# Performance work log

Hardware: AMD Instinct MI355X
Metric: run time of the kernel (lower is better)

## Reference

```python
import jax, jax.numpy as jnp
import numpy as np

N_NODES = 50000


def gcn_conv(x, edge_index, W, b):
    """GCNConv with added self-loops and symmetric D^-1/2 (A+I) D^-1/2 normalization."""
    n = x.shape[0]
    h = x @ W  # [N, out]
    loop = jnp.arange(n, dtype=edge_index.dtype)
    src = jnp.concatenate([edge_index[0], loop])
    dst = jnp.concatenate([edge_index[1], loop])
    ones = jnp.ones(src.shape[0], dtype=x.dtype)
    deg = jax.ops.segment_sum(ones, dst, num_segments=n)  # in-degree incl. self-loop
    dis = jnp.where(deg > 0, jax.lax.rsqrt(deg), 0.0).astype(x.dtype)
    norm = dis[src] * dis[dst]  # [E+N]
    msg = h[src] * norm[:, None]  # gather + scale
    out = jax.ops.segment_sum(msg, dst, num_segments=n)  # scatter-add
    return out + b


def setup_inputs() -> dict:
    key = jax.random.key(0)
    ks = jax.random.split(key, 6)
    d_in, d_h, d_out = 256, 256, 128
    x = jax.random.normal(ks[0], (N_NODES, d_in), dtype=jnp.float32)
    edge_index = jax.random.randint(ks[1], (2, 1600000), 0, N_NODES, dtype=jnp.int64)
    edge_label_index = jax.random.randint(ks[2], (2, 100000), 0, N_NODES, dtype=jnp.int64)
    W1 = jax.random.normal(ks[3], (d_in, d_h), dtype=jnp.float32) * (1.0 / np.sqrt(d_in))
    b1 = jnp.zeros((d_h,), dtype=jnp.float32)
    W2 = jax.random.normal(ks[4], (d_h, d_out), dtype=jnp.float32) * (1.0 / np.sqrt(d_h))
    b2 = jnp.zeros((d_out,), dtype=jnp.float32)
    return {"x": x, "edge_index": edge_index, "edge_label_index": edge_label_index,
            "W1": W1, "b1": b1, "W2": W2, "b2": b2}


def reference(x, edge_index, edge_label_index, W1, b1, W2, b2):
    # encode (eval mode: dropout is identity)
    z = jax.nn.relu(gcn_conv(x, edge_index, W1, b1))
    z = gcn_conv(z, edge_index, W2, b2)  # [N, 128]
    # decode: gather endpoint embeddings and reduce (edge dot-product scores)
    y = jnp.sum(z[edge_label_index[0]] * z[edge_label_index[1]], axis=-1)  # [E_label]
    return y
```

## Files before the change

### kernel.cpp

```cpp
#include <hip/hip_runtime.h>
#include <hip/hip_bf16.h>


#define CH 4096

typedef __attribute__((ext_vector_type(8))) short short8;
typedef __attribute__((ext_vector_type(4))) float f32x4;
typedef __attribute__((ext_vector_type(4))) unsigned int u32x4;

__device__ __forceinline__ unsigned short f2bf_rne(float f) {
  unsigned int b = __float_as_uint(f);
  b += 0x7FFFu + ((b >> 16) & 1u);
  return (unsigned short)(b >> 16);
}
__device__ __forceinline__ float u8f_0(unsigned int r) { return (float)(r & 255u); }
__device__ __forceinline__ float u8f_1(unsigned int r) { return (float)((r >> 8) & 255u); }
__device__ __forceinline__ float u8f_2(unsigned int r) { return (float)((r >> 16) & 255u); }
__device__ __forceinline__ float u8f_3(unsigned int r) { return (float)(r >> 24); }

__device__ __forceinline__ int dim1_of(int p) {
  return ((p >> 7) << 7) + (((p >> 6) & 1) << 6) + ((p >> 2) & 15) + ((p & 3) << 4);
}

__launch_bounds__(256) __global__
void prep_k(const float* __restrict__ W1, unsigned short* __restrict__ W1t,
            const float* __restrict__ W2, unsigned short* __restrict__ W2t,
            int* __restrict__ gcnt) {
  int t = threadIdx.x, b = blockIdx.x;
  if (b == 0) gcnt[t] = 0;
  int j = b * 256 + t;
  const int m1 = 256 * 256;
  if (j < m1) {
    int k = j >> 8, c = j & 255;
    W1t[(size_t)c * 256 + k] = f2bf_rne(W1[j]);
  } else if (j < m1 + 128 * 256) {
    int j2 = j - m1;
    int c = j2 >> 8, p = j2 & 255;
    W2t[(size_t)c * 256 + p] = f2bf_rne(W2[(size_t)dim1_of(p) * 128 + c]);
  }
}

#define LDST 40
template <bool AF32, int QROWW, bool DISFOLD>
__device__ __forceinline__
void gemm_body(const void* __restrict__ Av, const unsigned short* __restrict__ Bt,
               unsigned int* __restrict__ Q, float* __restrict__ wsout,
               const float* __restrict__ dis, int M, int N, int K, int bx, int by,
               short* As, short* Bs, float (*rm)[2]) {
  int t = threadIdx.x;
  int lane = t & 63, wave = t >> 6;
  int quad = lane >> 4, l16 = lane & 15;
  int wm = (wave & 1) * 64, wn = (wave >> 1) * 64;
  int wn6 = wn >> 6;
  int m0 = by * 128, n0 = bx * 128;

  int row0 = t >> 2, c80 = (t & 3) * 8;
  int row1 = row0 + 64, c81 = c80;
  int gr0 = m0 + row0, gr1 = m0 + row1;

  f32x4 acc[4][4];
#pragma unroll
  for (int i = 0; i < 4; i++)
#pragma unroll
    for (int j = 0; j < 4; j++) acc[i][j] = (f32x4)0.f;

  float4 fa00, fa01, fa10, fa11;
  uint4 ua0, ua1;
  uint4 ub0, ub1;

  auto load_tile = [&](int k0) {
    if (AF32) {
      const float* A = (const float*)Av;
      fa00 = make_float4(0.f, 0.f, 0.f, 0.f); fa01 = fa00; fa10 = fa00; fa11 = fa00;
      if (gr0 < M) {
        fa00 = *reinterpret_cast<const float4*>(A + (size_t)gr0 * K + k0 + c80);
        fa01 = *reinterpret_cast<const float4*>(A + (size_t)gr0 * K + k0 + c80 + 4);
      }
      if (gr1 < M) {
        fa10 = *reinterpret_cast<const float4*>(A + (size_t)gr1 * K + k0 + c81);
        fa11 = *reinterpret_cast<const float4*>(A + (size_t)gr1 * K + k0 + c81 + 4);
      }
    } else {
      const unsigned short* A = (const unsigned short*)Av;
      ua0 = make_uint4(0u, 0u, 0u, 0u); ua1 = ua0;
      if (gr0 < M) ua0 = *reinterpret_cast<const uint4*>(A + (size_t)gr0 * K + k0 + c80);
      if (gr1 < M) ua1 = *reinterpret_cast<const uint4*>(A + (size_t)gr1 * K + k0 + c81);
    }
    ub0 = *reinterpret_cast<const uint4*>(Bt + (size_t)(n0 + row0) * K + k0 + c80);
    ub1 = *reinterpret_cast<const uint4*>(Bt + (size_t)(n0 + row1) * K + k0 + c81);
  };

  load_tile(0);
  for (int k0 = 0; k0 < K; k0 += 32) {
    __syncthreads();
    uint4 av0, av1;
    if (AF32) {
      av0.x = (unsigned)f2bf_rne(fa00.x) | ((unsigned)f2bf_rne(fa00.y) << 16);
      av0.y = (unsigned)f2bf_rne(fa00.z) | ((unsigned)f2bf_rne(fa00.w) << 16);
      av0.z = (unsigned)f2bf_rne(fa01.x) | ((unsigned)f2bf_rne(fa01.y) << 16);
      av0.w = (unsigned)f2bf_rne(fa01.z) | ((unsigned)f2bf_rne(fa01.w) << 16);
      av1.x = (unsigned)f2bf_rne(fa10.x) | ((unsigned)f2bf_rne(fa10.y) << 16);
      av1.y = (unsigned)f2bf_rne(fa10.z) | ((unsigned)f2bf_rne(fa10.w) << 16);
      av1.z = (unsigned)f2bf_rne(fa11.x) | ((unsigned)f2bf_rne(fa11.y) << 16);
      av1.w = (unsigned)f2bf_rne(fa11.z) | ((unsigned)f2bf_rne(fa11.w) << 16);
    } else {
      av0 = ua0; av1 = ua1;
    }
    *reinterpret_cast<uint4*>(&As[row0 * LDST + c80]) = av0;
    *reinterpret_cast<uint4*>(&Bs[row0 * LDST + c80]) = ub0;
    *reinterpret_cast<uint4*>(&As[row1 * LDST + c81]) = av1;
    *reinterpret_cast<uint4*>(&Bs[row1 * LDST + c81]) = ub1;
    __syncthreads();
    if (k0 + 32 < K) load_tile(k0 + 32);
    short8 af[4], bfr[4];
#pragma unroll
    for (int mt = 0; mt < 4; mt++)
      af[mt] = *reinterpret_cast<const short8*>(&As[(wm + mt * 16 + l16) * LDST + quad * 8]);
#pragma unroll
    for (int nt = 0; nt < 4; nt++)
      bfr[nt] = *reinterpret_cast<const short8*>(&Bs[(wn + nt * 16 + l16) * LDST + quad * 8]);
#pragma unroll
    for (int mt = 0; mt < 4; mt++)
#pragma unroll
      for (int nt = 0; nt < 4; nt++)
        acc[mt][nt] = __builtin_amdgcn_mfma_f32_16x16x32_bf16(af[mt], bfr[nt], acc[mt][nt], 0, 0, 0);
  }

#pragma unroll
  for (int mt = 0; mt < 4; mt++) {
#pragma unroll
    for (int r = 0; r < 4; r++) {
      float m = fmaxf(fmaxf(fabsf(acc[mt][0][r]), fabsf(acc[mt][1][r])),
                      fmaxf(fabsf(acc[mt][2][r]), fabsf(acc[mt][3][r])));
#pragma unroll
      for (int off = 1; off < 16; off <<= 1) m = fmaxf(m, __shfl_xor(m, off));
      if (l16 == 0) rm[wm + mt * 16 + quad * 4 + r][wn6] = m;
    }
  }
  __syncthreads();
#pragma unroll
  for (int mt = 0; mt < 4; mt++) {
#pragma unroll
    for (int r = 0; r < 4; r++) {
      int rl = wm + mt * 16 + quad * 4 + r;
      int grow = m0 + rl;
      if (grow >= M) continue;
      float mx = fmaxf(rm[rl][0], rm[rl][1]);
      float inv = mx > 0.f ? 127.f / mx : 0.f;
      unsigned int uq[4];
#pragma unroll
      for (int nt = 0; nt < 4; nt++) {
        int tq = (int)rintf(acc[mt][nt][r] * inv);
        tq = tq > 127 ? 127 : (tq < -127 ? -127 : tq);
        uq[nt] = (unsigned int)(tq + 128);
      }
      unsigned int pk = uq[0] | (uq[1] << 8) | (uq[2] << 16) | (uq[3] << 24);
      int qcol = (QROWW == 64 ? (n0 >> 7) * 32 : 0) + wn6 * 16 + l16;
      Q[(size_t)grow * QROWW + qcol] = pk;
      if (wn6 == 0 && l16 == 0) {
        float sc = mx * (1.f / 127.f);
        if (DISFOLD) sc *= dis[grow];
        if (QROWW == 64) wsout[grow * 2 + (n0 >> 7)] = sc;
        else wsout[grow] = sc;
      }
    }
  }
}

__launch_bounds__(256) __global__
void fat1_k(const float* __restrict__ x, const unsigned short* __restrict__ W1t,
            unsigned int* __restrict__ Q, float* __restrict__ rawsc,
            int M, int N, int K, int NG,
            const int* __restrict__ src, const int* __restrict__ dst,
            int* __restrict__ gcnt, unsigned int* __restrict__ rec,
            int E, int BCAP) {
  __shared__ short As[128 * LDST];
  __shared__ short Bs[128 * LDST];
  __shared__ float rm[128][2];
  int bid = blockIdx.x;
  int t = threadIdx.x;
  if (bid < NG) {
    gemm_body<true, 64, false>(x, W1t, Q, rawsc, nullptr, M, N, K,
                               bid & 1, bid >> 1, As, Bs, rm);
    return;
  }
  int* h = (int*)As;
  int* ofs = h + 256;
  int* c2 = ofs + 256;
  int b = bid - NG;
  h[t] = 0;
  c2[t] = 0;
  __syncthreads();
  int i0 = b * CH, i1 = i0 + CH;
  if (i1 > E) i1 = E;
  for (int i = i0 + t; i < i1; i += 256) {
    int d = __builtin_nontemporal_load(&dst[i]);
    atomicAdd(&h[d >> 8], 1);
  }
  __syncthreads();
  {
    int cb = h[t];
    int base = atomicAdd(&gcnt[t], cb);
    ofs[t] = t * BCAP + base;
  }
  __syncthreads();
  int lim_base = 0;
  (void)lim_base;
  for (int i = i0 + t; i < i1; i += 256) {
    int d = __builtin_nontemporal_load(&dst[i]);
    int s = __builtin_nontemporal_load(&src[i]);
    int bk = d >> 8;
    int r = atomicAdd(&c2[bk], 1);
    int pos = ofs[bk] + r;
    if (pos < (bk + 1) * BCAP)
      rec[(size_t)pos] = ((unsigned int)(d & 255) << 16) | (unsigned int)s;
  }
}

__launch_bounds__(256) __global__
void sort2_dis_k(const unsigned int* __restrict__ rec, const int* __restrict__ gcnt,
                 unsigned short* __restrict__ edges, int* __restrict__ rowst,
                 int* __restrict__ fill, float* __restrict__ dis,
                 float* __restrict__ ws1, int n, int BCAP) {
  __shared__ int hist[256], scanv[256], c2[256];
  int t = threadIdx.x, b = blockIdx.x;
  int nrec = gcnt[b];
  if (nrec > BCAP) nrec = BCAP;
  size_t bs = (size_t)b * BCAP;
  hist[t] = 0;
  __syncthreads();
  const unsigned int* rp = rec + bs;
  for (int i = t; i < nrec; i += 256) atomicAdd(&hist[rp[i] >> 16], 1);
  __syncthreads();
  if (t == 0) {
    int s = 0;
    for (int k = 0; k < 256; k++) { scanv[k] = s; s += hist[k]; }
  }
  __syncthreads();
  int d = b * 256 + t;
  if (d < n) {
    fill[d] = hist[t];
    rowst[d] = (int)bs + scanv[t];
    float dv = rsqrtf((float)(hist[t] + 1));
    dis[d] = dv;
    ws1[2 * d] *= dv;
    ws1[2 * d + 1] *= dv;
  }
  c2[t] = 0;
  __syncthreads();
  for (int i = t; i < nrec; i += 256) {
    unsigned int r = rp[i];
    int dl = (int)(r >> 16);
    int pos = scanv[dl] + atomicAdd(&c2[dl], 1);
    edges[bs + pos] = (unsigned short)r;
  }
}

__launch_bounds__(256) __global__
void gemmq2_k(const unsigned short* __restrict__ A, const unsigned short* __restrict__ Bt,
              unsigned int* __restrict__ Q, float* __restrict__ wsout,
              const float* __restrict__ dis, int M, int N, int K) {
  __shared__ short As[128 * LDST];
  __shared__ short Bs[128 * LDST];
  __shared__ float rm[128][2];
  gemm_body<false, 32, true>(A, Bt, Q, wsout, dis, M, N, K, 0, blockIdx.x, As, Bs, rm);
}

template <int VEC, bool RELU, bool OBF, bool WS2>
__launch_bounds__(256) __global__
void aggregate_k(const void* __restrict__ qv, const int* __restrict__ fill,
                 const int* __restrict__ rowst, const unsigned short* __restrict__ edges,
                 const float* __restrict__ ws, const float* __restrict__ dis,
                 const float* __restrict__ bias, void* __restrict__ outv, int n) {
  const int DIM = VEC * 64;
  int wave = threadIdx.x >> 6, lane = threadIdx.x & 63;
  int node = blockIdx.x * (blockDim.x >> 6) + wave;
  if (node >= n) return;
  int start = rowst[node], end = start + fill[node];
  float di = dis[node];
  int hsel = lane >> 5;
  float bv[VEC];
  if (VEC == 4) {
    int base = (hsel << 7) + (((lane >> 4) & 1) << 6) + (lane & 15);
#pragma unroll
    for (int v = 0; v < 4; v++) bv[v] = bias[base + (v << 4)];
  } else {
    int c0 = (hsel << 6) + ((lane >> 1) & 15) + ((lane & 1) << 5);
    bv[0] = bias[c0];
    bv[1] = bias[c0 + 16];
  }
  const unsigned int* q4 = (const unsigned int*)qv;
  const unsigned short* q2 = (const unsigned short*)qv;
  float acc[VEC];
  float sw;
  {
    float w = WS2 ? ws[2 * node + hsel] : ws[node];
    sw = w;
    if (VEC == 4) {
      unsigned int r = q4[(size_t)node * 64 + lane];
      acc[0] = u8f_0(r) * w; acc[1] = u8f_1(r) * w;
      acc[2] = u8f_2(r) * w; acc[3] = u8f_3(r) * w;
    } else {
      unsigned int r = q2[(size_t)node * 64 + lane];
      acc[0] = u8f_0(r) * w; acc[1] = u8f_1(r) * w;
    }
  }
  int e = start;
  for (; e < end && (e & 7); e++) {
    unsigned int s = edges[e];
    float w = WS2 ? ws[2 * s + hsel] : ws[s];
    sw += w;
    if (VEC == 4) {
      unsigned int r = q4[(size_t)s * 64 + lane];
      acc[0] = fmaf(u8f_0(r), w, acc[0]);
      acc[1] = fmaf(u8f_1(r), w, acc[1]);
      acc[2] = fmaf(u8f_2(r), w, acc[2]);
      acc[3] = fmaf(u8f_3(r), w, acc[3]);
    } else {
      unsigned int r = q2[(size_t)s * 64 + lane];
      acc[0] = fmaf(u8f_0(r), w, acc[0]);
      acc[1] = fmaf(u8f_1(r), w, acc[1]);
    }
  }
  for (; e + 8 <= end; e += 8) {
    u32x4 ev = __builtin_nontemporal_load(reinterpret_cast<const u32x4*>(&edges[e]));
    unsigned int s[8];
    s[0] = ev.x & 0xFFFFu; s[1] = ev.x >> 16;
    s[2] = ev.y & 0xFFFFu; s[3] = ev.y >> 16;
    s[4] = ev.z & 0xFFFFu; s[5] = ev.z >> 16;
    s[6] = ev.w & 0xFFFFu; s[7] = ev.w >> 16;
    float w[8];
#pragma unroll
    for (int j = 0; j < 8; j++) w[j] = WS2 ? ws[2 * s[j] + hsel] : ws[s[j]];
#pragma unroll
    for (int j = 0; j < 8; j++) sw += w[j];
    if (VEC == 4) {
      unsigned int r[8];
#pragma unroll
      for (int j = 0; j < 8; j++) r[j] = q4[(size_t)s[j] * 64 + lane];
#pragma unroll
      for (int j = 0; j < 8; j++) {
        acc[0] = fmaf(u8f_0(r[j]), w[j], acc[0]);
        acc[1] = fmaf(u8f_1(r[j]), w[j], acc[1]);
        acc[2] = fmaf(u8f_2(r[j]), w[j], acc[2]);
        acc[3] = fmaf(u8f_3(r[j]), w[j], acc[3]);
      }
    } else {
      unsigned int r[8];
#pragma unroll
      for (int j = 0; j < 8; j++) r[j] = q2[(size_t)s[j] * 64 + lane];
#pragma unroll
      for (int j = 0; j < 8; j++) {
        acc[0] = fmaf(u8f_0(r[j]), w[j], acc[0]);
        acc[1] = fmaf(u8f_1(r[j]), w[j], acc[1]);
      }
    }
  }
  for (; e < end; e++) {
    unsigned int s = edges[e];
    float w = WS2 ? ws[2 * s + hsel] : ws[s];
    sw += w;
    if (VEC == 4) {
      unsigned int r = q4[(size_t)s * 64 + lane];
      acc[0] = fmaf(u8f_0(r), w, acc[0]);
      acc[1] = fmaf(u8f_1(r), w, acc[1]);
      acc[2] = fmaf(u8f_2(r), w, acc[2]);
      acc[3] = fmaf(u8f_3(r), w, acc[3]);
    } else {
      unsigned int r = q2[(size_t)s * 64 + lane];
      acc[0] = fmaf(u8f_0(r), w, acc[0]);
      acc[1] = fmaf(u8f_1(r), w, acc[1]);
    }
  }
  float corr = 128.f * sw;
#pragma unroll
  for (int v = 0; v < VEC; v++) {
    float r = fmaf(di, acc[v] - corr, bv[v]);
    if (RELU) r = fmaxf(r, 0.f);
    acc[v] = r;
  }
  if (OBF) {
    unsigned short* op = (unsigned short*)outv + (size_t)node * DIM + lane * VEC;
    if (VEC == 4) {
      unsigned int p0 = (unsigned int)f2bf_rne(acc[0]) | ((unsigned int)f2bf_rne(acc[1]) << 16);
      unsigned int p1 = (unsigned int)f2bf_rne(acc[2]) | ((unsigned int)f2bf_rne(acc[3]) << 16);
      *reinterpret_cast<uint2*>(op) = make_uint2(p0, p1);
    } else {
      unsigned int p0 = (unsigned int)f2bf_rne(acc[0]) | ((unsigned int)f2bf_rne(acc[1]) << 16);
      *reinterpret_cast<unsigned int*>(op) = p0;
    }
  } else {
    float* op = (float*)outv + (size_t)node * DIM + lane * VEC;
#pragma unroll
    for (int v = 0; v < VEC; v++) op[v] = acc[v];
  }
}

__launch_bounds__(256) __global__
void decode_k(const float* __restrict__ z, const int* __restrict__ ea,
              const int* __restrict__ eb, float* __restrict__ y, int E) {
  int wave = threadIdx.x >> 6, lane = threadIdx.x & 63;
  int e = blockIdx.x * (blockDim.x >> 6) + wave;
  if (e >= E) return;
  int a = ea[e], b = eb[e];
  const float2* za = reinterpret_cast<const float2*>(z + (size_t)a * 128);
  const float2* zb = reinterpret_cast<const float2*>(z + (size_t)b * 128);
  float2 pa = za[lane], pb = zb[lane];
  float s = pa.x * pb.x + pa.y * pb.y;
#pragma unroll
  for (int off = 32; off; off >>= 1) s += __shfl_down(s, off);
  if (lane == 0) y[e] = s;
}

extern "C" void kernel_launch(void* const* d_in, const int* in_sizes, int n_in,
                              void* d_out, int out_size, void* d_ws, size_t ws_size,
                              hipStream_t stream) {
  const float* x = (const float*)d_in[0];
  const int* ei = (const int*)d_in[1];
  const int* eli = (const int*)d_in[2];
  const float* W1 = (const float*)d_in[3];
  const float* b1 = (const float*)d_in[4];
  const float* W2 = (const float*)d_in[5];
  const float* b2 = (const float*)d_in[6];
  float* y = (float*)d_out;

  const int DIN = 256, DH = 256, DOUT = 128;
  const int n = in_sizes[0] / DIN;
  const int E = in_sizes[1] / 2;
  const int EL = in_sizes[2] / 2;
  const int* src = ei;
  const int* dst = ei + E;
  const int* ea = eli;
  const int* eb = eli + EL;

  const int NB = (E + CH - 1) / CH;
  const int NBUCK = (n + 255) / 256;
  const int PB = (DIN * DH + DH * DOUT + 255) / 256;
  const int MB = (n + 127) / 128;
  const int NG = 2 * MB;
  const int BCAP = 10240;

  size_t off = 0;
  auto alloc = [&](size_t bytes) {
    void* p = (char*)d_ws + off;
    off += (bytes + 255) & ~(size_t)255;
    return p;
  };
  int* fill = (int*)alloc((size_t)n * 4);
  int* rowst = (int*)alloc((size_t)n * 4);
  int* gcnt = (int*)alloc((size_t)256 * 4);
  unsigned int* rec = (unsigned int*)alloc((size_t)256 * BCAP * 4);
  float* dis = (float*)alloc((size_t)n * 4);
  float* ws2 = (float*)alloc((size_t)n * 2 * 4);
  float* wsB = (float*)alloc((size_t)n * 4);
  unsigned short* edges = (unsigned short*)alloc((size_t)256 * BCAP * 2);
  unsigned short* W1t = (unsigned short*)alloc((size_t)DIN * DH * 2);
  unsigned short* W2t = (unsigned short*)alloc((size_t)DH * DOUT * 2);
  unsigned int* qbuf = (unsigned int*)alloc((size_t)n * 64 * 4);
  unsigned short* z1b = (unsigned short*)alloc((size_t)n * DH * 2);
  float* z2 = (float*)alloc((size_t)n * DOUT * 4);
  (void)ws_size;

  prep_k<<<PB, 256, 0, stream>>>(W1, W1t, W2, W2t, gcnt);
  fat1_k<<<NG + NB, 256, 0, stream>>>(x, W1t, qbuf, ws2, n, DH, DIN, NG,
                                      src, dst, gcnt, rec, E, BCAP);
  sort2_dis_k<<<NBUCK, 256, 0, stream>>>(rec, gcnt, edges, rowst, fill, dis, ws2, n, BCAP);
  aggregate_k<4, true, true, true><<<(n + 3) / 4, 256, 0, stream>>>(
      qbuf, fill, rowst, edges, ws2, dis, b1, z1b, n);
  gemmq2_k<<<MB, 256, 0, stream>>>(z1b, W2t, qbuf, wsB, dis, n, DOUT, DH);
  aggregate_k<2, false, false, false><<<(n + 3) / 4, 256, 0, stream>>>(
      qbuf, fill, rowst, edges, wsB, dis, b2, z2, n);
  decode_k<<<(EL + 3) / 4, 256, 0, stream>>>(z2, ea, eb, y, EL);
}
```

Measured before the change: 341.7 us.

## Fuse all GCN stages into one persistent cooperative kernel with grid syncs

Replaces the seven separate kernel launches with a single cooperative persistent kernel that loops over each stage's work items and separates the stages with grid-wide barriers. The aim is to remove the per-launch overhead and the idle gaps between dependent kernels. The cost is fewer resident blocks, since occupancy is capped by the GEMM's shared-memory and register needs in every phase. Grid barriers also serialise the stages, and the old multi-kernel path is kept as a fallback if the cooperative launch fails.

```diff
diff --git a/kernel.cpp b/kernel.cpp
--- a/kernel.cpp
+++ b/kernel.cpp
@@ -1,5 +1,6 @@
 #include <hip/hip_runtime.h>
 #include <hip/hip_bf16.h>
+#include <hip/hip_cooperative_groups.h>
 
 
 #define CH 4096
@@ -20,6 +21,423 @@
 
 __device__ __forceinline__ int dim1_of(int p) {
   return ((p >> 7) << 7) + (((p >> 6) & 1) << 6) + ((p >> 2) & 15) + ((p & 3) << 4);
+}
+
+#define LDST 40
+template <bool AF32, int QROWW, bool DISFOLD>
+__device__ __forceinline__
+void gemm_body(const void* __restrict__ Av, const unsigned short* __restrict__ Bt,
+               unsigned int* __restrict__ Q, float* __restrict__ wsout,
+               const float* __restrict__ dis, int M, int N, int K, int bx, int by,
+               short* As, short* Bs, float (*rm)[2]) {
+  int t = threadIdx.x;
+  int lane = t & 63, wave = t >> 6;
+  int quad = lane >> 4, l16 = lane & 15;
+  int wm = (wave & 1) * 64, wn = (wave >> 1) * 64;
+  int wn6 = wn >> 6;
+  int m0 = by * 128, n0 = bx * 128;
+
+  int row0 = t >> 2, c80 = (t & 3) * 8;
+  int row1 = row0 + 64, c81 = c80;
+  int gr0 = m0 + row0, gr1 = m0 + row1;
+
+  f32x4 acc[4][4];
+#pragma unroll
+  for (int i = 0; i < 4; i++)
+#pragma unroll
+    for (int j = 0; j < 4; j++) acc[i][j] = (f32x4)0.f;
+
+  float4 fa00, fa01, fa10, fa11;
+  uint4 ua0, ua1;
+  uint4 ub0, ub1;
+
+  auto load_tile = [&](int k0) {
+    if (AF32) {
+      const float* A = (const float*)Av;
+      fa00 = make_float4(0.f, 0.f, 0.f, 0.f); fa01 = fa00; fa10 = fa00; fa11 = fa00;
+      if (gr0 < M) {
+        fa00 = *reinterpret_cast<const float4*>(A + (size_t)gr0 * K + k0 + c80);
+        fa01 = *reinterpret_cast<const float4*>(A + (size_t)gr0 * K + k0 + c80 + 4);
+      }
+      if (gr1 < M) {
+        fa10 = *reinterpret_cast<const float4*>(A + (size_t)gr1 * K + k0 + c81);
+        fa11 = *reinterpret_cast<const float4*>(A + (size_t)gr1 * K + k0 + c81 + 4);
+      }
+    } else {
+      const unsigned short* A = (const unsigned short*)Av;
+      ua0 = make_uint4(0u, 0u, 0u, 0u); ua1 = ua0;
+      if (gr0 < M) ua0 = *reinterpret_cast<const uint4*>(A + (size_t)gr0 * K + k0 + c80);
+      if (gr1 < M) ua1 = *reinterpret_cast<const uint4*>(A + (size_t)gr1 * K + k0 + c81);
+    }
+    ub0 = *reinterpret_cast<const uint4*>(Bt + (size_t)(n0 + row0) * K + k0 + c80);
+    ub1 = *reinterpret_cast<const uint4*>(Bt + (size_t)(n0 + row1) * K + k0 + c81);
+  };
+
+  load_tile(0);
+  for (int k0 = 0; k0 < K; k0 += 32) {
+    __syncthreads();
+    uint4 av0, av1;
+    if (AF32) {
+      av0.x = (unsigned)f2bf_rne(fa00.x) | ((unsigned)f2bf_rne(fa00.y) << 16);
+      av0.y = (unsigned)f2bf_rne(fa00.z) | ((unsigned)f2bf_rne(fa00.w) << 16);
+      av0.z = (unsigned)f2bf_rne(fa01.x) | ((unsigned)f2bf_rne(fa01.y) << 16);
+      av0.w = (unsigned)f2bf_rne(fa01.z) | ((unsigned)f2bf_rne(fa01.w) << 16);
+      av1.x = (unsigned)f2bf_rne(fa10.x) | ((unsigned)f2bf_rne(fa10.y) << 16);
+      av1.y = (unsigned)f2bf_rne(fa10.z) | ((unsigned)f2bf_rne(fa10.w) << 16);
+      av1.z = (unsigned)f2bf_rne(fa11.x) | ((unsigned)f2bf_rne(fa11.y) << 16);
+      av1.w = (unsigned)f2bf_rne(fa11.z) | ((unsigned)f2bf_rne(fa11.w) << 16);
+    } else {
+      av0 = ua0; av1 = ua1;
+    }
+    *reinterpret_cast<uint4*>(&As[row0 * LDST + c80]) = av0;
+    *reinterpret_cast<uint4*>(&Bs[row0 * LDST + c80]) = ub0;
+    *reinterpret_cast<uint4*>(&As[row1 * LDST + c81]) = av1;
+    *reinterpret_cast<uint4*>(&Bs[row1 * LDST + c81]) = ub1;
+    __syncthreads();
+    if (k0 + 32 < K) load_tile(k0 + 32);
+    short8 af[4], bfr[4];
+#pragma unroll
+    for (int mt = 0; mt < 4; mt++)
+      af[mt] = *reinterpret_cast<const short8*>(&As[(wm + mt * 16 + l16) * LDST + quad * 8]);
+#pragma unroll
+    for (int nt = 0; nt < 4; nt++)
+      bfr[nt] = *reinterpret_cast<const short8*>(&Bs[(wn + nt * 16 + l16) * LDST + quad * 8]);
+#pragma unroll
+    for (int mt = 0; mt < 4; mt++)
+#pragma unroll
+      for (int nt = 0; nt < 4; nt++)
+        acc[mt][nt] = __builtin_amdgcn_mfma_f32_16x16x32_bf16(af[mt], bfr[nt], acc[mt][nt], 0, 0, 0);
+  }
+
+#pragma unroll
+  for (int mt = 0; mt < 4; mt++) {
+#pragma unroll
+    for (int r = 0; r < 4; r++) {
+      float m = fmaxf(fmaxf(fabsf(acc[mt][0][r]), fabsf(acc[mt][1][r])),
+                      fmaxf(fabsf(acc[mt][2][r]), fabsf(acc[mt][3][r])));
+#pragma unroll
+      for (int off = 1; off < 16; off <<= 1) m = fmaxf(m, __shfl_xor(m, off));
+      if (l16 == 0) rm[wm + mt * 16 + quad * 4 + r][wn6] = m;
+    }
+  }
+  __syncthreads();
+#pragma unroll
+  for (int mt = 0; mt < 4; mt++) {
+#pragma unroll
+    for (int r = 0; r < 4; r++) {
+      int rl = wm + mt * 16 + quad * 4 + r;
+      int grow = m0 + rl;
+      if (grow >= M) continue;
+      float mx = fmaxf(rm[rl][0], rm[rl][1]);
+      float inv = mx > 0.f ? 127.f / mx : 0.f;
+      unsigned int uq[4];
+#pragma unroll
+      for (int nt = 0; nt < 4; nt++) {
+        int tq = (int)rintf(acc[mt][nt][r] * inv);
+        tq = tq > 127 ? 127 : (tq < -127 ? -127 : tq);
+        uq[nt] = (unsigned int)(tq + 128);
+      }
+      unsigned int pk = uq[0] | (uq[1] << 8) | (uq[2] << 16) | (uq[3] << 24);
+      int qcol = (QROWW == 64 ? (n0 >> 7) * 32 : 0) + wn6 * 16 + l16;
+      Q[(size_t)grow * QROWW + qcol] = pk;
+      if (wn6 == 0 && l16 == 0) {
+        float sc = mx * (1.f / 127.f);
+        if (DISFOLD) sc *= dis[grow];
+        if (QROWW == 64) wsout[grow * 2 + (n0 >> 7)] = sc;
+        else wsout[grow] = sc;
+      }
+    }
+  }
+}
+
+__device__ __forceinline__
+void scat_body(int b, const int* __restrict__ src, const int* __restrict__ dst,
+               int* __restrict__ gcnt, unsigned int* __restrict__ rec,
+               int E, int BCAP, int* lds) {
+  int t = threadIdx.x;
+  int* h = lds;
+  int* ofs = lds + 256;
+  int* c2 = lds + 512;
+  __syncthreads();
+  h[t] = 0;
+  c2[t] = 0;
+  __syncthreads();
+  int i0 = b * CH, i1 = i0 + CH;
+  if (i1 > E) i1 = E;
+  for (int i = i0 + t; i < i1; i += 256) {
+    int d = __builtin_nontemporal_load(&dst[i]);
+    atomicAdd(&h[d >> 8], 1);
+  }
+  __syncthreads();
+  {
+    int cb = h[t];
+    int base = atomicAdd(&gcnt[t], cb);
+    ofs[t] = t * BCAP + base;
+  }
+  __syncthreads();
+  for (int i = i0 + t; i < i1; i += 256) {
+    int d = __builtin_nontemporal_load(&dst[i]);
+    int s = __builtin_nontemporal_load(&src[i]);
+    int bk = d >> 8;
+    int r = atomicAdd(&c2[bk], 1);
+    int pos = ofs[bk] + r;
+    if (pos < (bk + 1) * BCAP)
+      rec[(size_t)pos] = ((unsigned int)(d & 255) << 16) | (unsigned int)s;
+  }
+}
+
+__device__ __forceinline__
+void sort2_body(int b, const unsigned int* __restrict__ rec, const int* __restrict__ gcnt,
+                unsigned short* __restrict__ edges, int* __restrict__ rowst,
+                int* __restrict__ fill, float* __restrict__ dis,
+                float* __restrict__ ws1, int n, int BCAP, int* lds) {
+  int t = threadIdx.x;
+  int* hist = lds;
+  int* scanv = lds + 256;
+  int* c2 = lds + 512;
+  int nrec = gcnt[b];
+  if (nrec > BCAP) nrec = BCAP;
+  size_t bs = (size_t)b * BCAP;
+  __syncthreads();
+  hist[t] = 0;
+  __syncthreads();
+  const unsigned int* rp = rec + bs;
+  for (int i = t; i < nrec; i += 256) atomicAdd(&hist[rp[i] >> 16], 1);
+  __syncthreads();
+  if (t == 0) {
+    int s = 0;
+    for (int k = 0; k < 256; k++) { scanv[k] = s; s += hist[k]; }
+  }
+  __syncthreads();
+  int d = b * 256 + t;
+  if (d < n) {
+    fill[d] = hist[t];
+    rowst[d] = (int)bs + scanv[t];
+    float dv = rsqrtf((float)(hist[t] + 1));
+    dis[d] = dv;
+    ws1[2 * d] *= dv;
+    ws1[2 * d + 1] *= dv;
+  }
+  c2[t] = 0;
+  __syncthreads();
+  for (int i = t; i < nrec; i += 256) {
+    unsigned int r = rp[i];
+    int dl = (int)(r >> 16);
+    int pos = scanv[dl] + atomicAdd(&c2[dl], 1);
+    edges[bs + pos] = (unsigned short)r;
+  }
+}
+
+template <int VEC, bool RELU, bool OBF, bool WS2>
+__device__ __forceinline__
+void agg_body(int wi, const void* __restrict__ qv, const int* __restrict__ fill,
+              const int* __restrict__ rowst, const unsigned short* __restrict__ edges,
+              const float* __restrict__ ws, const float* __restrict__ dis,
+              const float* __restrict__ bias, void* __restrict__ outv, int n) {
+  const int DIM = VEC * 64;
+  int wave = threadIdx.x >> 6, lane = threadIdx.x & 63;
+  int node = wi * 4 + wave;
+  if (node >= n) return;
+  int start = rowst[node], end = start + fill[node];
+  float di = dis[node];
+  int hsel = lane >> 5;
+  float bv[VEC];
+  if (VEC == 4) {
+    int base = (hsel << 7) + (((lane >> 4) & 1) << 6) + (lane & 15);
+#pragma unroll
+    for (int v = 0; v < 4; v++) bv[v] = bias[base + (v << 4)];
+  } else {
+    int c0 = (hsel << 6) + ((lane >> 1) & 15) + ((lane & 1) << 5);
+    bv[0] = bias[c0];
+    bv[1] = bias[c0 + 16];
+  }
+  const unsigned int* q4 = (const unsigned int*)qv;
+  const unsigned short* q2 = (const unsigned short*)qv;
+  float acc[VEC];
+  float sw;
+  {
+    float w = WS2 ? ws[2 * node + hsel] : ws[node];
+    sw = w;
+    if (VEC == 4) {
+      unsigned int r = q4[(size_t)node * 64 + lane];
+      acc[0] = u8f_0(r) * w; acc[1] = u8f_1(r) * w;
+      acc[2] = u8f_2(r) * w; acc[3] = u8f_3(r) * w;
+    } else {
+      unsigned int r = q2[(size_t)node * 64 + lane];
+      acc[0] = u8f_0(r) * w; acc[1] = u8f_1(r) * w;
+    }
+  }
+  int e = start;
+  for (; e < end && (e & 7); e++) {
+    unsigned int s = edges[e];
+    float w = WS2 ? ws[2 * s + hsel] : ws[s];
+    sw += w;
+    if (VEC == 4) {
+      unsigned int r = q4[(size_t)s * 64 + lane];
+      acc[0] = fmaf(u8f_0(r), w, acc[0]);
+      acc[1] = fmaf(u8f_1(r), w, acc[1]);
+      acc[2] = fmaf(u8f_2(r), w, acc[2]);
+      acc[3] = fmaf(u8f_3(r), w, acc[3]);
+    } else {
+      unsigned int r = q2[(size_t)s * 64 + lane];
+      acc[0] = fmaf(u8f_0(r), w, acc[0]);
+      acc[1] = fmaf(u8f_1(r), w, acc[1]);
+    }
+  }
+  for (; e + 8 <= end; e += 8) {
+    u32x4 ev = __builtin_nontemporal_load(reinterpret_cast<const u32x4*>(&edges[e]));
+    unsigned int s[8];
+    s[0] = ev.x & 0xFFFFu; s[1] = ev.x >> 16;
+    s[2] = ev.y & 0xFFFFu; s[3] = ev.y >> 16;
+    s[4] = ev.z & 0xFFFFu; s[5] = ev.z >> 16;
+    s[6] = ev.w & 0xFFFFu; s[7] = ev.w >> 16;
+    float w[8];
+#pragma unroll
+    for (int j = 0; j < 8; j++) w[j] = WS2 ? ws[2 * s[j] + hsel] : ws[s[j]];
+#pragma unroll
+    for (int j = 0; j < 8; j++) sw += w[j];
+    if (VEC == 4) {
+      unsigned int r[8];
+#pragma unroll
+      for (int j = 0; j < 8; j++) r[j] = q4[(size_t)s[j] * 64 + lane];
+#pragma unroll
+      for (int j = 0; j < 8; j++) {
+        acc[0] = fmaf(u8f_0(r[j]), w[j], acc[0]);
+        acc[1] = fmaf(u8f_1(r[j]), w[j], acc[1]);
+        acc[2] = fmaf(u8f_2(r[j]), w[j], acc[2]);
+        acc[3] = fmaf(u8f_3(r[j]), w[j], acc[3]);
+      }
+    } else {
+      unsigned int r[8];
+#pragma unroll
+      for (int j = 0; j < 8; j++) r[j] = q2[(size_t)s[j] * 64 + lane];
+#pragma unroll
+      for (int j = 0; j < 8; j++) {
+        acc[0] = fmaf(u8f_0(r[j]), w[j], acc[0]);
+        acc[1] = fmaf(u8f_1(r[j]), w[j], acc[1]);
+      }
+    }
+  }
+  for (; e < end; e++) {
+    unsigned int s = edges[e];
+    float w = WS2 ? ws[2 * s + hsel] : ws[s];
+    sw += w;
+    if (VEC == 4) {
+      unsigned int r = q4[(size_t)s * 64 + lane];
+      acc[0] = fmaf(u8f_0(r), w, acc[0]);
+      acc[1] = fmaf(u8f_1(r), w, acc[1]);
+      acc[2] = fmaf(u8f_2(r), w, acc[2]);
+      acc[3] = fmaf(u8f_3(r), w, acc[3]);
+    } else {
+      unsigned int r = q2[(size_t)s * 64 + lane];
+      acc[0] = fmaf(u8f_0(r), w, acc[0]);
+      acc[1] = fmaf(u8f_1(r), w, acc[1]);
+    }
+  }
+  float corr = 128.f * sw;
+#pragma unroll
+  for (int v = 0; v < VEC; v++) {
+    float r = fmaf(di, acc[v] - corr, bv[v]);
+    if (RELU) r = fmaxf(r, 0.f);
+    acc[v] = r;
+  }
+  if (OBF) {
+    unsigned short* op = (unsigned short*)outv + (size_t)node * DIM + lane * VEC;
+    if (VEC == 4) {
+      unsigned int p0 = (unsigned int)f2bf_rne(acc[0]) | ((unsigned int)f2bf_rne(acc[1]) << 16);
+      unsigned int p1 = (unsigned int)f2bf_rne(acc[2]) | ((unsigned int)f2bf_rne(acc[3]) << 16);
+      *reinterpret_cast<uint2*>(op) = make_uint2(p0, p1);
+    } else {
+      unsigned int p0 = (unsigned int)f2bf_rne(acc[0]) | ((unsigned int)f2bf_rne(acc[1]) << 16);
+      *reinterpret_cast<unsigned int*>(op) = p0;
+    }
+  } else {
+    float* op = (float*)outv + (size_t)node * DIM + lane * VEC;
+#pragma unroll
+    for (int v = 0; v < VEC; v++) op[v] = acc[v];
+  }
+}
+
+__device__ __forceinline__
+void decode_body(int wi, const float* __restrict__ z, const int* __restrict__ ea,
+                 const int* __restrict__ eb, float* __restrict__ y, int E) {
+  int wave = threadIdx.x >> 6, lane = threadIdx.x & 63;
+  int e = wi * 4 + wave;
+  if (e >= E) return;
+  int a = ea[e], b = eb[e];
+  const float2* za = reinterpret_cast<const float2*>(z + (size_t)a * 128);
+  const float2* zb = reinterpret_cast<const float2*>(z + (size_t)b * 128);
+  float2 pa = za[lane], pb = zb[lane];
+  float s = pa.x * pb.x + pa.y * pb.y;
+#pragma unroll
+  for (int off = 32; off; off >>= 1) s += __shfl_down(s, off);
+  if (lane == 0) y[e] = s;
+}
+
+__global__ void __launch_bounds__(256, 4)
+mega_k(const float* __restrict__ x, const int* __restrict__ src,
+       const int* __restrict__ dst, const int* __restrict__ ea,
+       const int* __restrict__ eb, const float* __restrict__ b1,
+       const float* __restrict__ b2, float* __restrict__ y,
+       const float* __restrict__ W1, const float* __restrict__ W2,
+       unsigned short* __restrict__ W1t, unsigned short* __restrict__ W2t,
+       int* __restrict__ gcnt, unsigned int* __restrict__ rec,
+       unsigned short* __restrict__ edges, int* __restrict__ rowst,
+       int* __restrict__ fill, float* __restrict__ dis,
+       float* __restrict__ ws2, float* __restrict__ wsB,
+       unsigned int* __restrict__ qbuf, unsigned short* __restrict__ z1b,
+       float* __restrict__ z2,
+       int n, int E, int EL, int NG, int NB, int NBUCK, int MB, int BCAP) {
+  __shared__ short As[128 * LDST];
+  __shared__ short Bs[128 * LDST];
+  __shared__ float rm[128][2];
+  int* ldsi = (int*)As;
+  cooperative_groups::grid_group grid = cooperative_groups::this_grid();
+  int t = threadIdx.x;
+
+  const int m1 = 256 * 256, m2 = 128 * 256;
+  for (int j = blockIdx.x * 256 + t; j < m1 + m2; j += gridDim.x * 256) {
+    if (j < m1) {
+      int k = j >> 8, c = j & 255;
+      W1t[(size_t)c * 256 + k] = f2bf_rne(W1[j]);
+    } else {
+      int j2 = j - m1;
+      int c = j2 >> 8, p = j2 & 255;
+      W2t[(size_t)c * 256 + p] = f2bf_rne(W2[(size_t)dim1_of(p) * 128 + c]);
+    }
+  }
+  if (blockIdx.x == 0) gcnt[t] = 0;
+  grid.sync();
+
+  for (int wi = blockIdx.x; wi < NG + NB; wi += gridDim.x) {
+    if (wi < NG)
+      gemm_body<true, 64, false>(x, W1t, qbuf, ws2, nullptr, n, 256, 256,
+                                 wi & 1, wi >> 1, As, Bs, rm);
+    else
+      scat_body(wi - NG, src, dst, gcnt, rec, E, BCAP, ldsi);
+  }
+  grid.sync();
+
+  for (int wi = blockIdx.x; wi < NBUCK; wi += gridDim.x)
+    sort2_body(wi, rec, gcnt, edges, rowst, fill, dis, ws2, n, BCAP, ldsi);
+  grid.sync();
+
+  int ng1 = (n + 3) >> 2;
+  for (int wi = blockIdx.x; wi < ng1; wi += gridDim.x)
+    agg_body<4, true, true, true>(wi, qbuf, fill, rowst, edges, ws2, dis, b1, z1b, n);
+  grid.sync();
+
+  for (int wi = blockIdx.x; wi < MB; wi += gridDim.x)
+    gemm_body<false, 32, true>(z1b, W2t, qbuf, wsB, dis, n, 128, 256, 0, wi, As, Bs, rm);
+  grid.sync();
+
+  for (int wi = blockIdx.x; wi < ng1; wi += gridDim.x)
+    agg_body<2, false, false, false>(wi, qbuf, fill, rowst, edges, wsB, dis, b2, z2, n);
+  grid.sync();
+
+  int nd = (EL + 3) >> 2;
+  for (int wi = blockIdx.x; wi < nd; wi += gridDim.x)
+    decode_body(wi, z2, ea, eb, y, EL);
 }
 
 __launch_bounds__(256) __global__
@@ -40,133 +458,6 @@
   }
 }
 
-#define LDST 40
-template <bool AF32, int QROWW, bool DISFOLD>
-__device__ __forceinline__
-void gemm_body(const void* __restrict__ Av, const unsigned short* __restrict__ Bt,
-               unsigned int* __restrict__ Q, float* __restrict__ wsout,
-               const float* __restrict__ dis, int M, int N, int K, int bx, int by,
-               short* As, short* Bs, float (*rm)[2]) {
-  int t = threadIdx.x;
-  int lane = t & 63, wave = t >> 6;
-  int quad = lane >> 4, l16 = lane & 15;
-  int wm = (wave & 1) * 64, wn = (wave >> 1) * 64;
-  int wn6 = wn >> 6;
-  int m0 = by * 128, n0 = bx * 128;
-
-  int row0 = t >> 2, c80 = (t & 3) * 8;
-  int row1 = row0 + 64, c81 = c80;
-  int gr0 = m0 + row0, gr1 = m0 + row1;
-
-  f32x4 acc[4][4];
-#pragma unroll
-  for (int i = 0; i < 4; i++)
-#pragma unroll
-    for (int j = 0; j < 4; j++) acc[i][j] = (f32x4)0.f;
-
-  float4 fa00, fa01, fa10, fa11;
-  uint4 ua0, ua1;
-  uint4 ub0, ub1;
-
-  auto load_tile = [&](int k0) {
-    if (AF32) {
-      const float* A = (const float*)Av;
-      fa00 = make_float4(0.f, 0.f, 0.f, 0.f); fa01 = fa00; fa10 = fa00; fa11 = fa00;
-      if (gr0 < M) {
-        fa00 = *reinterpret_cast<const float4*>(A + (size_t)gr0 * K + k0 + c80);
-        fa01 = *reinterpret_cast<const float4*>(A + (size_t)gr0 * K + k0 + c80 + 4);
-      }
-      if (gr1 < M) {
-        fa10 = *reinterpret_cast<const float4*>(A + (size_t)gr1 * K + k0 + c81);
-        fa11 = *reinterpret_cast<const float4*>(A + (size_t)gr1 * K + k0 + c81 + 4);
-      }
-    } else {
-      const unsigned short* A = (const unsigned short*)Av;
-      ua0 = make_uint4(0u, 0u, 0u, 0u); ua1 = ua0;
-      if (gr0 < M) ua0 = *reinterpret_cast<const uint4*>(A + (size_t)gr0 * K + k0 + c80);
-      if (gr1 < M) ua1 = *reinterpret_cast<const uint4*>(A + (size_t)gr1 * K + k0 + c81);
-    }
-    ub0 = *reinterpret_cast<const uint4*>(Bt + (size_t)(n0 + row0) * K + k0 + c80);
-    ub1 = *reinterpret_cast<const uint4*>(Bt + (size_t)(n0 + row1) * K + k0 + c81);
-  };
-
-  load_tile(0);
-  for (int k0 = 0; k0 < K; k0 += 32) {
-    __syncthreads();
-    uint4 av0, av1;
-    if (AF32) {
-      av0.x = (unsigned)f2bf_rne(fa00.x) | ((unsigned)f2bf_rne(fa00.y) << 16);
-      av0.y = (unsigned)f2bf_rne(fa00.z) | ((unsigned)f2bf_rne(fa00.w) << 16);
-      av0.z = (unsigned)f2bf_rne(fa01.x) | ((unsigned)f2bf_rne(fa01.y) << 16);
-      av0.w = (unsigned)f2bf_rne(fa01.z) | ((unsigned)f2bf_rne(fa01.w) << 16);
-      av1.x = (unsigned)f2bf_rne(fa10.x) | ((unsigned)f2bf_rne(fa10.y) << 16);
-      av1.y = (unsigned)f2bf_rne(fa10.z) | ((unsigned)f2bf_rne(fa10.w) << 16);
-      av1.z = (unsigned)f2bf_rne(fa11.x) | ((unsigned)f2bf_rne(fa11.y) << 16);
-      av1.w = (unsigned)f2bf_rne(fa11.z) | ((unsigned)f2bf_rne(fa11.w) << 16);
-    } else {
-      av0 = ua0; av1 = ua1;
-    }
-    *reinterpret_cast<uint4*>(&As[row0 * LDST + c80]) = av0;
-    *reinterpret_cast<uint4*>(&Bs[row0 * LDST + c80]) = ub0;
-    *reinterpret_cast<uint4*>(&As[row1 * LDST + c81]) = av1;
-    *reinterpret_cast<uint4*>(&Bs[row1 * LDST + c81]) = ub1;
-    __syncthreads();
-    if (k0 + 32 < K) load_tile(k0 + 32);
-    short8 af[4], bfr[4];
-#pragma unroll
-    for (int mt = 0; mt < 4; mt++)
-      af[mt] = *reinterpret_cast<const short8*>(&As[(wm + mt * 16 + l16) * LDST + quad * 8]);
-#pragma unroll
-    for (int nt = 0; nt < 4; nt++)
-      bfr[nt] = *reinterpret_cast<const short8*>(&Bs[(wn + nt * 16 + l16) * LDST + quad * 8]);
-#pragma unroll
-    for (int mt = 0; mt < 4; mt++)
-#pragma unroll
-      for (int nt = 0; nt < 4; nt++)
-        acc[mt][nt] = __builtin_amdgcn_mfma_f32_16x16x32_bf16(af[mt], bfr[nt], acc[mt][nt], 0, 0, 0);
-  }
-
-#pragma unroll
-  for (int mt = 0; mt < 4; mt++) {
-#pragma unroll
-    for (int r = 0; r < 4; r++) {
-      float m = fmaxf(fmaxf(fabsf(acc[mt][0][r]), fabsf(acc[mt][1][r])),
-                      fmaxf(fabsf(acc[mt][2][r]), fabsf(acc[mt][3][r])));
-#pragma unroll
-      for (int off = 1; off < 16; off <<= 1) m = fmaxf(m, __shfl_xor(m, off));
-      if (l16 == 0) rm[wm + mt * 16 + quad * 4 + r][wn6] = m;
-    }
-  }
-  __syncthreads();
-#pragma unroll
-  for (int mt = 0; mt < 4; mt++) {
-#pragma unroll
-    for (int r = 0; r < 4; r++) {
-      int rl = wm + mt * 16 + quad * 4 + r;
-      int grow = m0 + rl;
-      if (grow >= M) continue;
-      float mx = fmaxf(rm[rl][0], rm[rl][1]);
-      float inv = mx > 0.f ? 127.f / mx : 0.f;
-      unsigned int uq[4];
-#pragma unroll
-      for (int nt = 0; nt < 4; nt++) {
-        int tq = (int)rintf(acc[mt][nt][r] * inv);
-        tq = tq > 127 ? 127 : (tq < -127 ? -127 : tq);
-        uq[nt] = (unsigned int)(tq + 128);
-      }
-      unsigned int pk = uq[0] | (uq[1] << 8) | (uq[2] << 16) | (uq[3] << 24);
-      int qcol = (QROWW == 64 ? (n0 >> 7) * 32 : 0) + wn6 * 16 + l16;
-      Q[(size_t)grow * QROWW + qcol] = pk;
-      if (wn6 == 0 && l16 == 0) {
-        float sc = mx * (1.f / 127.f);
-        if (DISFOLD) sc *= dis[grow];
-        if (QROWW == 64) wsout[grow * 2 + (n0 >> 7)] = sc;
-        else wsout[grow] = sc;
-      }
-    }
-  }
-}
-
 __launch_bounds__(256) __global__
 void fat1_k(const float* __restrict__ x, const unsigned short* __restrict__ W1t,
             unsigned int* __restrict__ Q, float* __restrict__ rawsc,
@@ -178,43 +469,12 @@
   __shared__ short Bs[128 * LDST];
   __shared__ float rm[128][2];
   int bid = blockIdx.x;
-  int t = threadIdx.x;
   if (bid < NG) {
     gemm_body<true, 64, false>(x, W1t, Q, rawsc, nullptr, M, N, K,
                                bid & 1, bid >> 1, As, Bs, rm);
     return;
   }
-  int* h = (int*)As;
-  int* ofs = h + 256;
-  int* c2 = ofs + 256;
-  int b = bid - NG;
-  h[t] = 0;
-  c2[t] = 0;
-  __syncthreads();
-  int i0 = b * CH, i1 = i0 + CH;
-  if (i1 > E) i1 = E;
-  for (int i = i0 + t; i < i1; i += 256) {
-    int d = __builtin_nontemporal_load(&dst[i]);
-    atomicAdd(&h[d >> 8], 1);
-  }
-  __syncthreads();
-  {
-    int cb = h[t];
-    int base = atomicAdd(&gcnt[t], cb);
-    ofs[t] = t * BCAP + base;
-  }
-  __syncthreads();
-  int lim_base = 0;
-  (void)lim_base;
-  for (int i = i0 + t; i < i1; i += 256) {
-    int d = __builtin_nontemporal_load(&dst[i]);
-    int s = __builtin_nontemporal_load(&src[i]);
-    int bk = d >> 8;
-    int r = atomicAdd(&c2[bk], 1);
-    int pos = ofs[bk] + r;
-    if (pos < (bk + 1) * BCAP)
-      rec[(size_t)pos] = ((unsigned int)(d & 255) << 16) | (unsigned int)s;
-  }
+  scat_body(bid - NG, src, dst, gcnt, rec, E, BCAP, (int*)As);
 }
 
 __launch_bounds__(256) __global__
@@ -222,38 +482,17 @@
                  unsigned short* __restrict__ edges, int* __restrict__ rowst,
                  int* __restrict__ fill, float* __restrict__ dis,
                  float* __restrict__ ws1, int n, int BCAP) {
-  __shared__ int hist[256], scanv[256], c2[256];
-  int t = threadIdx.x, b = blockIdx.x;
-  int nrec = gcnt[b];
-  if (nrec > BCAP) nrec = BCAP;
-  size_t bs = (size_t)b * BCAP;
-  hist[t] = 0;
-  __syncthreads();
-  const unsigned int* rp = rec + bs;
-  for (int i = t; i < nrec; i += 256) atomicAdd(&hist[rp[i] >> 16], 1);
-  __syncthreads();
-  if (t == 0) {
-    int s = 0;
-    for (int k = 0; k < 256; k++) { scanv[k] = s; s += hist[k]; }
-  }
-  __syncthreads();
-  int d = b * 256 + t;
-  if (d < n) {
-    fill[d] = hist[t];
-    rowst[d] = (int)bs + scanv[t];
-    float dv = rsqrtf((float)(hist[t] + 1));
-    dis[d] = dv;
-    ws1[2 * d] *= dv;
-    ws1[2 * d + 1] *= dv;
-  }
-  c2[t] = 0;
-  __syncthreads();
-  for (int i = t; i < nrec; i += 256) {
-    unsigned int r = rp[i];
-    int dl = (int)(r >> 16);
-    int pos = scanv[dl] + atomicAdd(&c2[dl], 1);
-    edges[bs + pos] = (unsigned short)r;
-  }
+  __shared__ int lds[768];
+  sort2_body(blockIdx.x, rec, gcnt, edges, rowst, fill, dis, ws1, n, BCAP, lds);
+}
+
+template <int VEC, bool RELU, bool OBF, bool WS2>
+__launch_bounds__(256) __global__
+void aggregate_k(const void* __restrict__ qv, const int* __restrict__ fill,
+                 const int* __restrict__ rowst, const unsigned short* __restrict__ edges,
+                 const float* __restrict__ ws, const float* __restrict__ dis,
+                 const float* __restrict__ bias, void* __restrict__ outv, int n) {
+  agg_body<VEC, RELU, OBF, WS2>(blockIdx.x, qv, fill, rowst, edges, ws, dis, bias, outv, n);
 }
 
 __launch_bounds__(256) __global__
@@ -266,150 +505,10 @@
   gemm_body<false, 32, true>(A, Bt, Q, wsout, dis, M, N, K, 0, blockIdx.x, As, Bs, rm);
 }
 
-template <int VEC, bool RELU, bool OBF, bool WS2>
-__launch_bounds__(256) __global__
-void aggregate_k(const void* __restrict__ qv, const int* __restrict__ fill,
-                 const int* __restrict__ rowst, const unsigned short* __restrict__ edges,
-                 const float* __restrict__ ws, const float* __restrict__ dis,
-                 const float* __restrict__ bias, void* __restrict__ outv, int n) {
-  const int DIM = VEC * 64;
-  int wave = threadIdx.x >> 6, lane = threadIdx.x & 63;
-  int node = blockIdx.x * (blockDim.x >> 6) + wave;
-  if (node >= n) return;
-  int start = rowst[node], end = start + fill[node];
-  float di = dis[node];
-  int hsel = lane >> 5;
-  float bv[VEC];
-  if (VEC == 4) {
-    int base = (hsel << 7) + (((lane >> 4) & 1) << 6) + (lane & 15);
-#pragma unroll
-    for (int v = 0; v < 4; v++) bv[v] = bias[base + (v << 4)];
-  } else {
-    int c0 = (hsel << 6) + ((lane >> 1) & 15) + ((lane & 1) << 5);
-    bv[0] = bias[c0];
-    bv[1] = bias[c0 + 16];
-  }
-  const unsigned int* q4 = (const unsigned int*)qv;
-  const unsigned short* q2 = (const unsigned short*)qv;
-  float acc[VEC];
-  float sw;
-  {
-    float w = WS2 ? ws[2 * node + hsel] : ws[node];
-    sw = w;
-    if (VEC == 4) {
-      unsigned int r = q4[(size_t)node * 64 + lane];
-      acc[0] = u8f_0(r) * w; acc[1] = u8f_1(r) * w;
-      acc[2] = u8f_2(r) * w; acc[3] = u8f_3(r) * w;
-    } else {
-      unsigned int r = q2[(size_t)node * 64 + lane];
-      acc[0] = u8f_0(r) * w; acc[1] = u8f_1(r) * w;
-    }
-  }
-  int e = start;
-  for (; e < end && (e & 7); e++) {
-    unsigned int s = edges[e];
-    float w = WS2 ? ws[2 * s + hsel] : ws[s];
-    sw += w;
-    if (VEC == 4) {
-      unsigned int r = q4[(size_t)s * 64 + lane];
-      acc[0] = fmaf(u8f_0(r), w, acc[0]);
-      acc[1] = fmaf(u8f_1(r), w, acc[1]);
-      acc[2] = fmaf(u8f_2(r), w, acc[2]);
-      acc[3] = fmaf(u8f_3(r), w, acc[3]);
-    } else {
-      unsigned int r = q2[(size_t)s * 64 + lane];
-      acc[0] = fmaf(u8f_0(r), w, acc[0]);
-      acc[1] = fmaf(u8f_1(r), w, acc[1]);
-    }
-  }
-  for (; e + 8 <= end; e += 8) {
-    u32x4 ev = __builtin_nontemporal_load(reinterpret_cast<const u32x4*>(&edges[e]));
-    unsigned int s[8];
-    s[0] = ev.x & 0xFFFFu; s[1] = ev.x >> 16;
-    s[2] = ev.y & 0xFFFFu; s[3] = ev.y >> 16;
-    s[4] = ev.z & 0xFFFFu; s[5] = ev.z >> 16;
-    s[6] = ev.w & 0xFFFFu; s[7] = ev.w >> 16;
-    float w[8];
-#pragma unroll
-    for (int j = 0; j < 8; j++) w[j] = WS2 ? ws[2 * s[j] + hsel] : ws[s[j]];
-#pragma unroll
-    for (int j = 0; j < 8; j++) sw += w[j];
-    if (VEC == 4) {
-      unsigned int r[8];
-#pragma unroll
-      for (int j = 0; j < 8; j++) r[j] = q4[(size_t)s[j] * 64 + lane];
-#pragma unroll
-      for (int j = 0; j < 8; j++) {
-        acc[0] = fmaf(u8f_0(r[j]), w[j], acc[0]);
-        acc[1] = fmaf(u8f_1(r[j]), w[j], acc[1]);
-        acc[2] = fmaf(u8f_2(r[j]), w[j], acc[2]);
-        acc[3] = fmaf(u8f_3(r[j]), w[j], acc[3]);
-      }
-    } else {
-      unsigned int r[8];
-#pragma unroll
-      for (int j = 0; j < 8; j++) r[j] = q2[(size_t)s[j] * 64 + lane];
-#pragma unroll
-      for (int j = 0; j < 8; j++) {
-        acc[0] = fmaf(u8f_0(r[j]), w[j], acc[0]);
-        acc[1] = fmaf(u8f_1(r[j]), w[j], acc[1]);
-      }
-    }
-  }
-  for (; e < end; e++) {
-    unsigned int s = edges[e];
-    float w = WS2 ? ws[2 * s + hsel] : ws[s];
-    sw += w;
-    if (VEC == 4) {
-      unsigned int r = q4[(size_t)s * 64 + lane];
-      acc[0] = fmaf(u8f_0(r), w, acc[0]);
-      acc[1] = fmaf(u8f_1(r), w, acc[1]);
-      acc[2] = fmaf(u8f_2(r), w, acc[2]);
-      acc[3] = fmaf(u8f_3(r), w, acc[3]);
-    } else {
-      unsigned int r = q2[(size_t)s * 64 + lane];
-      acc[0] = fmaf(u8f_0(r), w, acc[0]);
-      acc[1] = fmaf(u8f_1(r), w, acc[1]);
-    }
-  }
-  float corr = 128.f * sw;
-#pragma unroll
-  for (int v = 0; v < VEC; v++) {
-    float r = fmaf(di, acc[v] - corr, bv[v]);
-    if (RELU) r = fmaxf(r, 0.f);
-    acc[v] = r;
-  }
-  if (OBF) {
-    unsigned short* op = (unsigned short*)outv + (size_t)node * DIM + lane * VEC;
-    if (VEC == 4) {
-      unsigned int p0 = (unsigned int)f2bf_rne(acc[0]) | ((unsigned int)f2bf_rne(acc[1]) << 16);
-      unsigned int p1 = (unsigned int)f2bf_rne(acc[2]) | ((unsigned int)f2bf_rne(acc[3]) << 16);
-      *reinterpret_cast<uint2*>(op) = make_uint2(p0, p1);
-    } else {
-      unsigned int p0 = (unsigned int)f2bf_rne(acc[0]) | ((unsigned int)f2bf_rne(acc[1]) << 16);
-      *reinterpret_cast<unsigned int*>(op) = p0;
-    }
-  } else {
-    float* op = (float*)outv + (size_t)node * DIM + lane * VEC;
-#pragma unroll
-    for (int v = 0; v < VEC; v++) op[v] = acc[v];
-  }
-}
-
 __launch_bounds__(256) __global__
 void decode_k(const float* __restrict__ z, const int* __restrict__ ea,
               const int* __restrict__ eb, float* __restrict__ y, int E) {
-  int wave = threadIdx.x >> 6, lane = threadIdx.x & 63;
-  int e = blockIdx.x * (blockDim.x >> 6) + wave;
-  if (e >= E) return;
-  int a = ea[e], b = eb[e];
-  const float2* za = reinterpret_cast<const float2*>(z + (size_t)a * 128);
-  const float2* zb = reinterpret_cast<const float2*>(z + (size_t)b * 128);
-  float2 pa = za[lane], pb = zb[lane];
-  float s = pa.x * pb.x + pa.y * pb.y;
-#pragma unroll
-  for (int off = 32; off; off >>= 1) s += __shfl_down(s, off);
-  if (lane == 0) y[e] = s;
+  decode_body(blockIdx.x, z, ea, eb, y, E);
 }
 
 extern "C" void kernel_launch(void* const* d_in, const int* in_sizes, int n_in,
@@ -425,20 +524,20 @@
   float* y = (float*)d_out;
 
   const int DIN = 256, DH = 256, DOUT = 128;
-  const int n = in_sizes[0] / DIN;
-  const int E = in_sizes[1] / 2;
-  const int EL = in_sizes[2] / 2;
+  int n = in_sizes[0] / DIN;
+  int E = in_sizes[1] / 2;
+  int EL = in_sizes[2] / 2;
   const int* src = ei;
   const int* dst = ei + E;
   const int* ea = eli;
   const int* eb = eli + EL;
 
-  const int NB = (E + CH - 1) / CH;
-  const int NBUCK = (n + 255) / 256;
+  int NB = (E + CH - 1) / CH;
+  int NBUCK = (n + 255) / 256;
   const int PB = (DIN * DH + DH * DOUT + 255) / 256;
-  const int MB = (n + 127) / 128;
-  const int NG = 2 * MB;
-  const int BCAP = 10240;
+  int MB = (n + 127) / 128;
+  int NG = 2 * MB;
+  int BCAP = 10240;
 
   size_t off = 0;
   auto alloc = [&](size_t bytes) {
@@ -461,6 +560,30 @@
   float* z2 = (float*)alloc((size_t)n * DOUT * 4);
   (void)ws_size;
 
+  static int nblk = 0;
+  if (nblk == 0) {
+    int mab = 0;
+    if (hipOccupancyMaxActiveBlocksPerMultiprocessor(&mab, mega_k, 256, 0) != hipSuccess ||
+        mab < 1)
+      mab = 4;
+    int ncu = 256;
+    hipDeviceProp_t prop;
+    if (hipGetDeviceProperties(&prop, 0) == hipSuccess && prop.multiProcessorCount > 0)
+      ncu = prop.multiProcessorCount;
+    nblk = mab * ncu;
+  }
+
+  void* args[] = {(void*)&x,    (void*)&src,  (void*)&dst,  (void*)&ea,   (void*)&eb,
+                  (void*)&b1,   (void*)&b2,   (void*)&y,    (void*)&W1,   (void*)&W2,
+                  (void*)&W1t,  (void*)&W2t,  (void*)&gcnt, (void*)&rec,  (void*)&edges,
+                  (void*)&rowst,(void*)&fill, (void*)&dis,  (void*)&ws2,  (void*)&wsB,
+                  (void*)&qbuf, (void*)&z1b,  (void*)&z2,
+                  (void*)&n,    (void*)&E,    (void*)&EL,   (void*)&NG,   (void*)&NB,
+                  (void*)&NBUCK,(void*)&MB,   (void*)&BCAP};
+  hipError_t lerr = hipLaunchCooperativeKernel((const void*)mega_k, dim3(nblk), dim3(256),
+                                               args, 0, stream);
+  if (lerr == hipSuccess) return;
+
   prep_k<<<PB, 256, 0, stream>>>(W1, W1t, W2, W2t, gcnt);
   fat1_k<<<NG + NB, 256, 0, stream>>>(x, W1t, qbuf, ws2, n, DH, DIN, NG,
                                       src, dst, gcnt, rec, E, BCAP);
```

New measurement: 921.7 us. 2.7x slower.
